# Performance work log

Measured on AMD Instinct MI355X. Metric: run time of the kernel, lower is better.

## Reference

```python
import jax, jax.numpy as jnp
import numpy as np

N = 100000        # nodes
E = 1600000       # edges (avg degree 16)
D_IN = 32
D_OUT = 64
K_HOPS = 2        # SGC propagation steps
CUTGRAPH = 0.1
K_CUT = int(E * CUTGRAPH)  # edges pruned per hop (lowest cosine similarity)
L2_EPS = 1e-12    # torch F.normalize eps


def setup_inputs() -> dict:
    key = jax.random.key(0)
    k1, k2, k3, k4 = jax.random.split(key, 4)
    features = jax.random.normal(k1, (N, D_IN), dtype=jnp.float32)
    src = jax.random.randint(k2, (E,), 0, N, dtype=jnp.int32)
    dst = jax.random.randint(k3, (E,), 0, N, dtype=jnp.int32)
    # fc weight (out_feats, in_feats), Xavier-uniform-like scale
    W = jax.random.normal(k4, (D_OUT, D_IN), dtype=jnp.float32) * (1.0 / np.sqrt(D_IN))
    return {"features": features, "src": src, "dst": dst, "W": W}


def reference(features, src, dst, W):
    # in-degree (messages flow src -> dst), clamped at 1
    deg = jax.ops.segment_sum(jnp.ones((E,), features.dtype), dst, num_segments=N)
    norm = jnp.power(jnp.clip(deg, 1.0, None), -0.5)[:, None]  # [N,1]

    h = features
    for _ in range(K_HOPS):
        # edge weights: ones, with bottom-K_CUT cosine-similarity edges zeroed
        nh = h / jnp.maximum(jnp.linalg.norm(h, axis=-1, keepdims=True), L2_EPS)
        cos = jnp.sum(nh[src] * nh[dst], axis=-1)               # [E]
        _, cut_idx = jax.lax.top_k(-cos, K_CUT)                 # smallest cos
        w = jnp.ones((E,), h.dtype).at[cut_idx].set(0.0)

        # symmetric degree-normalized propagation: D^-1/2 A D^-1/2 h
        h = h * norm
        msg = h[src] * w[:, None]                               # [E, D_IN]
        h = jax.ops.segment_sum(msg, dst, num_segments=N)       # [N, D_IN]
        h = h * norm

    return h @ W.T  # fc, no bias
```

## Files before the change

### kernel.cpp

```cpp
#include <hip/hip_runtime.h>


constexpr int NN   = 100000;
constexpr int NE   = 1600000;
constexpr int DI   = 32;
constexpr int DO   = 64;
constexpr int KCUT = 160000;
constexpr int NB   = 98;
constexpr int CH   = 4096;
constexpr int HB   = 256;
constexpr int SCAP = 19456;

typedef unsigned long long u64;


__global__ void k_zero_u32(unsigned* p, int n) {
  int i = blockIdx.x * blockDim.x + threadIdx.x;
  if (i < n) p[i] = 0u;
}

__global__ void k_norm(const unsigned* __restrict__ degi, float* __restrict__ nrm) {
  int i = blockIdx.x * blockDim.x + threadIdx.x;
  if (i < NN) {
    unsigned d = degi[i]; if (d < 1u) d = 1u;
    nrm[i] = (float)(1.0 / sqrt((double)d));
  }
}


__global__ void k_bhist(const int* __restrict__ dst, unsigned* __restrict__ bhist) {
  __shared__ unsigned lh[128];
  int t = threadIdx.x;
  if (t < 128) lh[t] = 0u;
  __syncthreads();
  int stride = gridDim.x * blockDim.x;
  for (int e = blockIdx.x * blockDim.x + t; e < NE; e += stride)
    atomicAdd(&lh[((unsigned)dst[e]) >> 10], 1u);
  __syncthreads();
  if (t < 128 && lh[t]) atomicAdd(&bhist[t], lh[t]);
}

__global__ void k_bscan(const unsigned* __restrict__ bhist, unsigned* __restrict__ bstart,
                        unsigned* __restrict__ bcur) {
  if (threadIdx.x == 0 && blockIdx.x == 0) {
    unsigned run = 0;
    for (int b = 0; b < NB; b++) { bstart[b] = run; bcur[b] = run; run += bhist[b]; }
    bstart[NB] = run;
  }
}

__global__ void k_bin(const int* __restrict__ src, const int* __restrict__ dst,
                      unsigned* __restrict__ bcur, u64* __restrict__ binned) {
  __shared__ unsigned h1[128], h2[128], res[128];
  int t = threadIdx.x;
  for (int base = blockIdx.x * CH; base < NE; base += gridDim.x * CH) {
    int nE = min(CH, NE - base);
    if (t < 128) h1[t] = 0u;
    __syncthreads();
    for (int i = t; i < nE; i += 256)
      atomicAdd(&h1[((unsigned)dst[base + i]) >> 10], 1u);
    __syncthreads();
    if (t < 128) { unsigned c = h1[t]; res[t] = c ? atomicAdd(&bcur[t], c) : 0u; h2[t] = 0u; }
    __syncthreads();
    for (int i = t; i < nE; i += 256) {
      unsigned d = (unsigned)dst[base + i];
      unsigned bb = d >> 10;
      u64 pk = ((u64)(d & 1023u) << 38) | ((u64)(unsigned)src[base + i] << 21)
             | (u64)(unsigned)(base + i);
      unsigned r = atomicAdd(&h2[bb], 1u);
      binned[res[bb] + r] = pk;
    }
    __syncthreads();
  }
}

__global__ void k_bucket_deg(const u64* __restrict__ binned, const unsigned* __restrict__ bstart,
                             unsigned* __restrict__ degi) {
  __shared__ unsigned cnt[1024];
  int t = threadIdx.x;
  int b = blockIdx.x;
  for (int i = t; i < 1024; i += 256) cnt[i] = 0u;
  __syncthreads();
  unsigned j0 = bstart[b], j1 = bstart[b + 1];
  for (unsigned j = j0 + t; j < j1; j += 256)
    atomicAdd(&cnt[(unsigned)(binned[j] >> 38)], 1u);
  __syncthreads();
  int base = b << 10;
  for (int i = t; i < 1024; i += 256)
    if (base + i < NN) degi[base + i] = cnt[i];
}

__global__ void k_bucket_scatter(const u64* __restrict__ binned, const unsigned* __restrict__ bstart,
                                 const unsigned* __restrict__ rowptr, uint2* __restrict__ csr) {
  extern __shared__ unsigned smem[];
  unsigned* curl = smem;
  u64* stage = (u64*)(smem + 1024);
  int t = threadIdx.x;
  int b = blockIdx.x;
  unsigned j0 = bstart[b], j1 = bstart[b + 1];
  int base = b << 10;
  for (int i = t; i < 1024; i += 256)
    curl[i] = (base + i < NN) ? (rowptr[base + i] - j0) : 0u;
  __syncthreads();
  for (unsigned j = j0 + t; j < j1; j += 256) {
    u64 pk = binned[j];
    unsigned dloc = (unsigned)(pk >> 38);
    unsigned s = (unsigned)((pk >> 21) & 0x1FFFFu);
    unsigned e = (unsigned)(pk & 0x1FFFFFu);
    unsigned p = atomicAdd(&curl[dloc], 1u);
    u64 entry = ((u64)e << 32) | (u64)s;
    if (p < (unsigned)SCAP) stage[p] = entry;
    else csr[j0 + p] = make_uint2(s, e);
  }
  __syncthreads();
  unsigned cnt = j1 - j0;
  u64* gout = (u64*)(csr + j0);
  for (unsigned i = t; i < cnt; i += 256)
    if (i < (unsigned)SCAP) gout[i] = stage[i];
}


__global__ void k_psum_a(const unsigned* __restrict__ degi, unsigned* __restrict__ bsum) {
  __shared__ unsigned s[1024];
  int t = threadIdx.x;
  int i = blockIdx.x * 1024 + t;
  s[t] = (i < NN) ? degi[i] : 0u;
  __syncthreads();
  for (int off = 512; off > 0; off >>= 1) {
    if (t < off) s[t] += s[t + off];
    __syncthreads();
  }
  if (t == 0) bsum[blockIdx.x] = s[0];
}

__global__ void k_psum_b(unsigned* bsum, int nb, unsigned* rowptr) {
  if (threadIdx.x == 0 && blockIdx.x == 0) {
    unsigned run = 0;
    for (int b = 0; b < nb; b++) { unsigned v = bsum[b]; bsum[b] = run; run += v; }
    rowptr[NN] = run;
  }
}

__global__ void k_psum_c(const unsigned* __restrict__ degi, const unsigned* __restrict__ bsum,
                         unsigned* __restrict__ rowptr) {
  __shared__ unsigned s[1024];
  int t = threadIdx.x;
  int i = blockIdx.x * 1024 + t;
  unsigned v = (i < NN) ? degi[i] : 0u;
  s[t] = v; __syncthreads();
  for (int off = 1; off < 1024; off <<= 1) {
    unsigned x = (t >= off) ? s[t - off] : 0u;
    __syncthreads();
    s[t] += x;
    __syncthreads();
  }
  if (i < NN) rowptr[i] = bsum[blockIdx.x] + s[t] - v;
}


__global__ void k_rownorm(const float* __restrict__ h, const float* __restrict__ nrm,
                          float* __restrict__ nh, float* __restrict__ hn) {
  int lane = threadIdx.x & 31;
  int n = blockIdx.x * 8 + (threadIdx.x >> 5);
  float v = h[n * DI + lane];
  double sq = (double)v * (double)v;
  #pragma unroll
  for (int m = 16; m > 0; m >>= 1) sq += __shfl_xor(sq, m, 32);
  double den = sqrt(sq);
  if (den < 1e-12) den = 1e-12;
  nh[n * DI + lane] = (float)((double)v / den);
  hn[n * DI + lane] = v * nrm[n];
}

__global__ void k_cos(const unsigned* __restrict__ rowptr, const uint2* __restrict__ csr,
                      const float* __restrict__ nh, u64* __restrict__ key) {
  int t = threadIdx.x;
  int lane = t & 31;
  int sl = lane >> 2;
  int ds = lane & 3;
  int n = blockIdx.x * 8 + (t >> 5);
  const float4* drow = (const float4*)(nh + (size_t)n * DI + ds * 8);
  float4 d0 = drow[0], d1 = drow[1];
  unsigned j0 = rowptr[n], j1 = rowptr[n + 1];
  for (unsigned base = j0; base < j1; base += 8) {
    unsigned j = base + sl;
    bool val = (j < j1);
    uint2 c = val ? csr[j] : make_uint2(0u, 0u);
    const float4* arow = (const float4*)(nh + (size_t)c.x * DI + ds * 8);
    float4 a0 = arow[0], a1 = arow[1];
    double p = (double)a0.x * d0.x + (double)a0.y * d0.y
             + (double)a0.z * d0.z + (double)a0.w * d0.w
             + (double)a1.x * d1.x + (double)a1.y * d1.y
             + (double)a1.z * d1.z + (double)a1.w * d1.w;
    p += __shfl_xor(p, 1, 32);
    p += __shfl_xor(p, 2, 32);
    if (val && ds == 0) {
      float cf = (float)p;
      unsigned u = __float_as_uint(cf);
      u = (u & 0x80000000u) ? ~u : (u | 0x80000000u);
      key[j] = ((u64)u << 32) | (u64)c.y;
    }
  }
}


__global__ void k_hist_big(const u64* __restrict__ keys, unsigned* __restrict__ ghist,
                           u64* state, unsigned* cur) {
  __shared__ unsigned lh[4096];
  int t = threadIdx.x;
  if (blockIdx.x == 0 && t == 0) {
    state[0] = 0ull; state[1] = (u64)KCUT; cur[0] = 0u; cur[1] = 0u;
  }
  for (int i = t; i < 4096; i += 256) lh[i] = 0u;
  __syncthreads();
  int stride = gridDim.x * blockDim.x;
  for (int j = blockIdx.x * blockDim.x + t; j < NE; j += stride)
    atomicAdd(&lh[(unsigned)(keys[j] >> 52)], 1u);
  __syncthreads();
  unsigned* gh = ghist + (size_t)blockIdx.x * 4096;
  for (int i = t; i < 4096; i += 256) gh[i] = lh[i];
}

__global__ void k_hist_reduce(const unsigned* __restrict__ ghist, unsigned* __restrict__ hist) {
  int bin = blockIdx.x * 256 + threadIdx.x;
  unsigned s = 0;
  for (int b = 0; b < HB; b++) s += ghist[(size_t)b * 4096 + bin];
  hist[bin] = s;
}

__global__ void k_hist(const u64* __restrict__ keys, const unsigned* __restrict__ cntp,
                       const u64* __restrict__ state,
                       unsigned* __restrict__ hist, int shift, int check) {
  __shared__ unsigned lh[4096];
  int t = threadIdx.x;
  for (int i = t; i < 4096; i += 256) lh[i] = 0u;
  __syncthreads();
  int n = (int)*cntp;
  u64 pref = state[0];
  int stride = gridDim.x * blockDim.x;
  for (int j = blockIdx.x * blockDim.x + t; j < n; j += stride) {
    u64 k = keys[j];
    bool ok = (check == 0) || (((k ^ pref) >> check) == 0ull);
    if (ok) atomicAdd(&lh[(unsigned)((k >> shift) & 4095ull)], 1u);
  }
  __syncthreads();
  for (int i = t; i < 4096; i += 256) if (lh[i]) atomicAdd(&hist[i], lh[i]);
}

__global__ void k_select(unsigned* hist, u64* state, int shift) {
  __shared__ unsigned ssum[256];
  int t = threadIdx.x;
  unsigned loc[16]; unsigned tot = 0;
  #pragma unroll
  for (int i = 0; i < 16; i++) { loc[i] = hist[t * 16 + i]; tot += loc[i]; }
  #pragma unroll
  for (int i = 0; i < 16; i++) hist[t * 16 + i] = 0u;
  unsigned krem = (unsigned)state[1];
  ssum[t] = tot; __syncthreads();
  for (int off = 1; off < 256; off <<= 1) {
    unsigned x = (t >= off) ? ssum[t - off] : 0u;
    __syncthreads();
    ssum[t] += x;
    __syncthreads();
  }
  unsigned incl = ssum[t], excl = incl - tot;
  if (incl >= krem && excl < krem) {
    unsigned run = excl; int b = 0; unsigned nk = 0;
    #pragma unroll
    for (int i = 0; i < 16; i++) {
      if (krem <= run + loc[i]) { b = t * 16 + i; nk = krem - run; break; }
      run += loc[i];
    }
    state[0] |= ((u64)b) << shift;
    state[1] = (u64)nk;
  }
}

__global__ void k_compact(const u64* __restrict__ keys, const unsigned* __restrict__ cntp,
                          int n_fixed, const u64* __restrict__ state, int check,
                          u64* __restrict__ outbuf, unsigned* __restrict__ cursor) {
  __shared__ u64 buf[768];
  __shared__ unsigned cnt, gbase;
  int t = threadIdx.x;
  if (t == 0) cnt = 0u;
  __syncthreads();
  int n = cntp ? (int)*cntp : n_fixed;
  u64 pref = state[0];
  int stride = gridDim.x * blockDim.x;
  for (int j0 = blockIdx.x * blockDim.x; j0 < n; j0 += stride) {
    int j = j0 + t;
    if (j < n) {
      u64 k = keys[j];
      if (((k ^ pref) >> check) == 0ull) {
        unsigned pos = atomicAdd(&cnt, 1u);
        buf[pos] = k;
      }
    }
    __syncthreads();
    if (cnt >= 512u) {
      if (t == 0) gbase = atomicAdd(cursor, cnt);
      __syncthreads();
      for (unsigned i = t; i < cnt; i += blockDim.x) outbuf[gbase + i] = buf[i];
      __syncthreads();
      if (t == 0) cnt = 0u;
      __syncthreads();
    }
  }
  if (t == 0 && cnt > 0u) gbase = atomicAdd(cursor, cnt);
  __syncthreads();
  for (unsigned i = t; i < cnt; i += blockDim.x) outbuf[gbase + i] = buf[i];
}

__global__ void __launch_bounds__(1024) k_finish(const u64* __restrict__ cb,
                                                 const unsigned* __restrict__ cur,
                                                 u64* __restrict__ state) {
  __shared__ unsigned h[1024];
  __shared__ u64 spref;
  __shared__ unsigned skrem;
  int t = threadIdx.x;
  unsigned cnt = cur[1];
  if (t == 0) { spref = state[0]; skrem = (unsigned)state[1]; }
  __syncthreads();
  for (int shift = 30; shift >= 0; shift -= 10) {
    h[t] = 0u; __syncthreads();
    u64 pref = spref;
    for (unsigned j = t; j < cnt; j += 1024) {
      u64 k = cb[j];
      if (((k ^ pref) >> (shift + 10)) == 0ull)
        atomicAdd(&h[(unsigned)((k >> shift) & 1023ull)], 1u);
    }
    __syncthreads();
    unsigned v = h[t];
    for (int off = 1; off < 1024; off <<= 1) {
      unsigned x = (t >= off) ? h[t - off] : 0u;
      __syncthreads();
      h[t] += x;
      __syncthreads();
    }
    unsigned incl = h[t], excl = incl - v;
    unsigned krem = skrem;
    __syncthreads();
    if (incl >= krem && excl < krem) {
      spref |= ((u64)t) << shift;
      skrem = krem - excl;
    }
    __syncthreads();
  }
  if (t == 0) state[0] = spref;
}


__global__ void k_prop(const unsigned* __restrict__ rowptr, const uint2* __restrict__ csr,
                       const u64* __restrict__ key, const u64* __restrict__ state,
                       const float* __restrict__ hn, const float* __restrict__ nrm,
                       float* __restrict__ hout) {
  int t = threadIdx.x;
  int lane = t & 31;
  int sl = lane >> 2, ds = lane & 3;
  int n = blockIdx.x * 8 + (t >> 5);
  u64 X = state[0];
  unsigned j0 = rowptr[n], j1 = rowptr[n + 1];
  double acc[8];
  #pragma unroll
  for (int i = 0; i < 8; i++) acc[i] = 0.0;
  for (unsigned base = j0; base < j1; base += 8) {
    unsigned j = base + sl;
    bool val = (j < j1);
    uint2 c = val ? csr[j] : make_uint2(0u, 0u);
    u64 k = val ? key[j] : 0ull;
    bool keep = val && (k > X);
    const float4* arow = (const float4*)(hn + (size_t)c.x * DI + ds * 8);
    float4 a0 = arow[0], a1 = arow[1];
    if (keep) {
      acc[0] += (double)a0.x; acc[1] += (double)a0.y;
      acc[2] += (double)a0.z; acc[3] += (double)a0.w;
      acc[4] += (double)a1.x; acc[5] += (double)a1.y;
      acc[6] += (double)a1.z; acc[7] += (double)a1.w;
    }
  }
  #pragma unroll
  for (int m = 4; m <= 16; m <<= 1) {
    #pragma unroll
    for (int i = 0; i < 8; i++) acc[i] += __shfl_xor(acc[i], m, 32);
  }
  if (sl == 0) {
    float nv = nrm[n];
    float4 o0, o1;
    o0.x = (float)acc[0] * nv; o0.y = (float)acc[1] * nv;
    o0.z = (float)acc[2] * nv; o0.w = (float)acc[3] * nv;
    o1.x = (float)acc[4] * nv; o1.y = (float)acc[5] * nv;
    o1.z = (float)acc[6] * nv; o1.w = (float)acc[7] * nv;
    float4* orow = (float4*)(hout + (size_t)n * DI + ds * 8);
    orow[0] = o0; orow[1] = o1;
  }
}


__global__ void k_fc(const float* __restrict__ h, const float* __restrict__ W,
                     float* __restrict__ out) {
  __shared__ float Wt[DI * 65];
  __shared__ float hs[4 * DI];
  int t = threadIdx.x;
  #pragma unroll
  for (int i = 0; i < 8; i++) {
    int idx = t + i * 256;
    Wt[(idx & 31) * 65 + (idx >> 5)] = W[idx];
  }
  int n0 = blockIdx.x * 4;
  if (t < 128) hs[t] = h[n0 * DI + t];
  __syncthreads();
  int o = t & 63, nl = t >> 6;
  float acc = 0.f;
  #pragma unroll
  for (int d = 0; d < DI; d++) acc += hs[nl * DI + d] * Wt[d * 65 + o];
  out[(n0 + nl) * DO + o] = acc;
}


extern "C" void kernel_launch(void* const* d_in, const int* in_sizes, int n_in,
                              void* d_out, int out_size, void* d_ws, size_t ws_size,
                              hipStream_t stream) {
  const float* feat = (const float*)d_in[0];
  const int*   src  = (const int*)d_in[1];
  const int*   dst  = (const int*)d_in[2];
  const float* W    = (const float*)d_in[3];
  float*       out  = (float*)d_out;

  float* bufA = (float*)d_ws;
  float* bufB = bufA + (size_t)NN * DI;
  float* bufC = bufB + (size_t)NN * DI;
  u64*   key  = (u64*)(bufC + (size_t)NN * DI);
  u64*   cbuf2 = key + NE;
  u64*   binned = cbuf2;
  unsigned* ghist = (unsigned*)cbuf2;
  float*    nrm     = (float*)(cbuf2 + NE);
  unsigned* degi    = (unsigned*)(nrm + NN);
  unsigned* rowptr  = degi + NN;
  unsigned* fill    = rowptr + NN + 2;
  unsigned* bsum    = fill + NN;
  unsigned* hist    = bsum + 128;
  unsigned* cur     = hist + 4096;
  u64*      state   = (u64*)(cur + 2);
  uint2*    csr     = (uint2*)(state + 2);
  unsigned* bhist   = (unsigned*)(csr + NE);
  unsigned* bstart  = bhist + 128;
  unsigned* bcur    = bstart + 100;

  k_zero_u32<<<1, 128, 0, stream>>>(bhist, 128);
  k_bhist<<<512, 256, 0, stream>>>(dst, bhist);
  k_bscan<<<1, 1, 0, stream>>>(bhist, bstart, bcur);
  k_bin<<<(NE + CH - 1) / CH, 256, 0, stream>>>(src, dst, bcur, binned);
  k_bucket_deg<<<NB, 256, 0, stream>>>(binned, bstart, degi);
  k_norm<<<(NN + 255) / 256, 256, 0, stream>>>(degi, nrm);
  int nb = (NN + 1023) / 1024;
  k_psum_a<<<nb, 1024, 0, stream>>>(degi, bsum);
  k_psum_b<<<1, 1, 0, stream>>>(bsum, nb, rowptr);
  k_psum_c<<<nb, 1024, 0, stream>>>(degi, bsum, rowptr);
  size_t scatter_lds = 1024 * sizeof(unsigned) + (size_t)SCAP * sizeof(u64);
  k_bucket_scatter<<<NB, 256, scatter_lds, stream>>>(binned, bstart, rowptr, csr);

  const float* hin = feat;
  for (int hop = 0; hop < 2; hop++) {
    float* nh = (hop == 0) ? bufA : bufC;
    float* hn = bufB;
    float* ho = (hop == 0) ? bufA : bufC;
    u64* cbuf1 = (u64*)((hop == 0) ? bufC : bufA);

    k_rownorm<<<NN / 8, 256, 0, stream>>>(hin, nrm, nh, hn);
    k_cos<<<NN / 8, 256, 0, stream>>>(rowptr, csr, nh, key);

    k_hist_big<<<HB, 256, 0, stream>>>(key, ghist, state, cur);
    k_hist_reduce<<<16, 256, 0, stream>>>(ghist, hist);
    k_select<<<1, 256, 0, stream>>>(hist, state, 52);
    k_compact<<<512, 256, 0, stream>>>(key, nullptr, NE, state, 52, cbuf1, cur + 0);
    k_hist<<<64, 256, 0, stream>>>(cbuf1, cur + 0, state, hist, 40, 0);
    k_select<<<1, 256, 0, stream>>>(hist, state, 40);
    k_compact<<<64, 256, 0, stream>>>(cbuf1, cur + 0, 0, state, 40, cbuf2, cur + 1);
    k_finish<<<1, 1024, 0, stream>>>(cbuf2, cur, state);

    k_prop<<<NN / 8, 256, 0, stream>>>(rowptr, csr, key, state, hn, nrm, ho);
    hin = ho;
  }
  k_fc<<<NN / 4, 256, 0, stream>>>(hin, W, out);
}
```

Before: 472.1 us.

## Cut kernel launches in radix top-k select and preprocessing via fused kernels

Merges the histogram reduce and first bucket select into one kernel using a last-block-done atomic, and drops the second histogram/select/compact pass. The remaining 52-bit prefix refinement now runs inside a single 1024-thread finish kernel over the first compacted buffer, in 12-bit rounds. Preprocessing also fuses the degree-norm computation into the prefix-sum kernel and replaces the atomic bucket histogram plus serial scan with per-block partials and a parallel scan. This removes several small launches and serial kernels. In exchange, one workgroup must now scan the whole first-level candidate set across five rounds, which could be slow if that set is large.

After: 512.5 us. 8.6% more time.

```diff
diff --git a/kernel.cpp b/kernel.cpp
--- a/kernel.cpp
+++ b/kernel.cpp
@@ -9,26 +9,13 @@
 constexpr int NB   = 98;
 constexpr int CH   = 4096;
 constexpr int HB   = 256;
+constexpr int HBH  = 512;
 constexpr int SCAP = 19456;
 
 typedef unsigned long long u64;
 
 
-__global__ void k_zero_u32(unsigned* p, int n) {
-  int i = blockIdx.x * blockDim.x + threadIdx.x;
-  if (i < n) p[i] = 0u;
-}
-
-__global__ void k_norm(const unsigned* __restrict__ degi, float* __restrict__ nrm) {
-  int i = blockIdx.x * blockDim.x + threadIdx.x;
-  if (i < NN) {
-    unsigned d = degi[i]; if (d < 1u) d = 1u;
-    nrm[i] = (float)(1.0 / sqrt((double)d));
-  }
-}
-
-
-__global__ void k_bhist(const int* __restrict__ dst, unsigned* __restrict__ bhist) {
+__global__ void k_bhist(const int* __restrict__ dst, unsigned* __restrict__ bpart) {
   __shared__ unsigned lh[128];
   int t = threadIdx.x;
   if (t < 128) lh[t] = 0u;
@@ -37,16 +24,25 @@
   for (int e = blockIdx.x * blockDim.x + t; e < NE; e += stride)
     atomicAdd(&lh[((unsigned)dst[e]) >> 10], 1u);
   __syncthreads();
-  if (t < 128 && lh[t]) atomicAdd(&bhist[t], lh[t]);
-}
-
-__global__ void k_bscan(const unsigned* __restrict__ bhist, unsigned* __restrict__ bstart,
-                        unsigned* __restrict__ bcur) {
-  if (threadIdx.x == 0 && blockIdx.x == 0) {
-    unsigned run = 0;
-    for (int b = 0; b < NB; b++) { bstart[b] = run; bcur[b] = run; run += bhist[b]; }
-    bstart[NB] = run;
-  }
+  if (t < 128) bpart[blockIdx.x * 128 + t] = lh[t];
+}
+
+__global__ void k_bscan2(const unsigned* __restrict__ bpart, unsigned* __restrict__ bstart,
+                         unsigned* __restrict__ bcur) {
+  __shared__ unsigned s[128];
+  int t = threadIdx.x;
+  unsigned sum = 0;
+  for (int b = 0; b < HBH; b++) sum += bpart[b * 128 + t];
+  s[t] = sum; __syncthreads();
+  for (int off = 1; off < 128; off <<= 1) {
+    unsigned x = (t >= off) ? s[t - off] : 0u;
+    __syncthreads();
+    s[t] += x;
+    __syncthreads();
+  }
+  unsigned incl = s[t], excl = incl - sum;
+  if (t < NB) { bstart[t] = excl; bcur[t] = excl; }
+  if (t == NB - 1) bstart[NB] = incl;
 }
 
 __global__ void k_bin(const int* __restrict__ src, const int* __restrict__ dst,
@@ -142,7 +138,7 @@
 }
 
 __global__ void k_psum_c(const unsigned* __restrict__ degi, const unsigned* __restrict__ bsum,
-                         unsigned* __restrict__ rowptr) {
+                         unsigned* __restrict__ rowptr, float* __restrict__ nrm) {
   __shared__ unsigned s[1024];
   int t = threadIdx.x;
   int i = blockIdx.x * 1024 + t;
@@ -154,7 +150,11 @@
     s[t] += x;
     __syncthreads();
   }
-  if (i < NN) rowptr[i] = bsum[blockIdx.x] + s[t] - v;
+  if (i < NN) {
+    rowptr[i] = bsum[blockIdx.x] + s[t] - v;
+    unsigned d = v < 1u ? 1u : v;
+    nrm[i] = (float)(1.0 / sqrt((double)d));
+  }
 }
 
 
@@ -209,7 +209,7 @@
   __shared__ unsigned lh[4096];
   int t = threadIdx.x;
   if (blockIdx.x == 0 && t == 0) {
-    state[0] = 0ull; state[1] = (u64)KCUT; cur[0] = 0u; cur[1] = 0u;
+    state[0] = 0ull; state[1] = (u64)KCUT; cur[0] = 0u; cur[1] = 0u; cur[2] = 0u;
   }
   for (int i = t; i < 4096; i += 256) lh[i] = 0u;
   __syncthreads();
@@ -221,40 +221,23 @@
   for (int i = t; i < 4096; i += 256) gh[i] = lh[i];
 }
 
-__global__ void k_hist_reduce(const unsigned* __restrict__ ghist, unsigned* __restrict__ hist) {
-  int bin = blockIdx.x * 256 + threadIdx.x;
+__global__ void k_hist_reduce_sel(const unsigned* __restrict__ ghist, unsigned* __restrict__ hist,
+                                  u64* state, unsigned* cur) {
+  __shared__ unsigned ssum[256];
+  __shared__ unsigned isLast;
+  int t = threadIdx.x;
+  int bin = blockIdx.x * 256 + t;
   unsigned s = 0;
   for (int b = 0; b < HB; b++) s += ghist[(size_t)b * 4096 + bin];
   hist[bin] = s;
-}
-
-__global__ void k_hist(const u64* __restrict__ keys, const unsigned* __restrict__ cntp,
-                       const u64* __restrict__ state,
-                       unsigned* __restrict__ hist, int shift, int check) {
-  __shared__ unsigned lh[4096];
-  int t = threadIdx.x;
-  for (int i = t; i < 4096; i += 256) lh[i] = 0u;
-  __syncthreads();
-  int n = (int)*cntp;
-  u64 pref = state[0];
-  int stride = gridDim.x * blockDim.x;
-  for (int j = blockIdx.x * blockDim.x + t; j < n; j += stride) {
-    u64 k = keys[j];
-    bool ok = (check == 0) || (((k ^ pref) >> check) == 0ull);
-    if (ok) atomicAdd(&lh[(unsigned)((k >> shift) & 4095ull)], 1u);
-  }
-  __syncthreads();
-  for (int i = t; i < 4096; i += 256) if (lh[i]) atomicAdd(&hist[i], lh[i]);
-}
-
-__global__ void k_select(unsigned* hist, u64* state, int shift) {
-  __shared__ unsigned ssum[256];
-  int t = threadIdx.x;
+  __threadfence();
+  if (t == 0) isLast = (atomicAdd(&cur[2], 1u) == gridDim.x - 1u) ? 1u : 0u;
+  __syncthreads();
+  if (!isLast) return;
+  __threadfence();
   unsigned loc[16]; unsigned tot = 0;
   #pragma unroll
   for (int i = 0; i < 16; i++) { loc[i] = hist[t * 16 + i]; tot += loc[i]; }
-  #pragma unroll
-  for (int i = 0; i < 16; i++) hist[t * 16 + i] = 0u;
   unsigned krem = (unsigned)state[1];
   ssum[t] = tot; __syncthreads();
   for (int off = 1; off < 256; off <<= 1) {
@@ -265,33 +248,33 @@
   }
   unsigned incl = ssum[t], excl = incl - tot;
   if (incl >= krem && excl < krem) {
-    unsigned run = excl; int b = 0; unsigned nk = 0;
+    unsigned run = excl;
     #pragma unroll
     for (int i = 0; i < 16; i++) {
-      if (krem <= run + loc[i]) { b = t * 16 + i; nk = krem - run; break; }
+      if (krem <= run + loc[i]) {
+        state[0] |= ((u64)(t * 16 + i)) << 52;
+        state[1] = (u64)(krem - run);
+        break;
+      }
       run += loc[i];
     }
-    state[0] |= ((u64)b) << shift;
-    state[1] = (u64)nk;
-  }
-}
-
-__global__ void k_compact(const u64* __restrict__ keys, const unsigned* __restrict__ cntp,
-                          int n_fixed, const u64* __restrict__ state, int check,
+  }
+}
+
+__global__ void k_compact(const u64* __restrict__ keys, const u64* __restrict__ state,
                           u64* __restrict__ outbuf, unsigned* __restrict__ cursor) {
   __shared__ u64 buf[768];
   __shared__ unsigned cnt, gbase;
   int t = threadIdx.x;
   if (t == 0) cnt = 0u;
   __syncthreads();
-  int n = cntp ? (int)*cntp : n_fixed;
   u64 pref = state[0];
   int stride = gridDim.x * blockDim.x;
-  for (int j0 = blockIdx.x * blockDim.x; j0 < n; j0 += stride) {
+  for (int j0 = blockIdx.x * blockDim.x; j0 < NE; j0 += stride) {
     int j = j0 + t;
-    if (j < n) {
+    if (j < NE) {
       u64 k = keys[j];
-      if (((k ^ pref) >> check) == 0ull) {
+      if (((k ^ pref) >> 52) == 0ull) {
         unsigned pos = atomicAdd(&cnt, 1u);
         buf[pos] = k;
       }
@@ -311,38 +294,58 @@
   for (unsigned i = t; i < cnt; i += blockDim.x) outbuf[gbase + i] = buf[i];
 }
 
-__global__ void __launch_bounds__(1024) k_finish(const u64* __restrict__ cb,
-                                                 const unsigned* __restrict__ cur,
-                                                 u64* __restrict__ state) {
-  __shared__ unsigned h[1024];
+__global__ void __launch_bounds__(1024) k_finish2(const u64* __restrict__ cb,
+                                                  const unsigned* __restrict__ cur,
+                                                  u64* __restrict__ state) {
+  __shared__ unsigned lh[4096];
+  __shared__ unsigned ssum[1024];
   __shared__ u64 spref;
   __shared__ unsigned skrem;
   int t = threadIdx.x;
-  unsigned cnt = cur[1];
+  unsigned cnt = cur[0];
   if (t == 0) { spref = state[0]; skrem = (unsigned)state[1]; }
   __syncthreads();
-  for (int shift = 30; shift >= 0; shift -= 10) {
-    h[t] = 0u; __syncthreads();
+  for (int r = 0; r < 5; r++) {
+    int shift = (r < 4) ? (40 - 12 * r) : 0;
+    int width = (r < 4) ? 12 : 4;
+    int nbins = 1 << width;
+    int check = shift + width;
+    for (int i = t; i < nbins; i += 1024) lh[i] = 0u;
+    __syncthreads();
     u64 pref = spref;
     for (unsigned j = t; j < cnt; j += 1024) {
       u64 k = cb[j];
-      if (((k ^ pref) >> (shift + 10)) == 0ull)
-        atomicAdd(&h[(unsigned)((k >> shift) & 1023ull)], 1u);
-    }
-    __syncthreads();
-    unsigned v = h[t];
+      if (((k ^ pref) >> check) == 0ull)
+        atomicAdd(&lh[(unsigned)((k >> shift) & (u64)(nbins - 1))], 1u);
+    }
+    __syncthreads();
+    int per = (nbins + 1023) / 1024;
+    unsigned loc[4]; unsigned tot = 0;
+    for (int i = 0; i < per; i++) {
+      int b = t * per + i;
+      loc[i] = (b < nbins) ? lh[b] : 0u;
+      tot += loc[i];
+    }
+    ssum[t] = tot; __syncthreads();
     for (int off = 1; off < 1024; off <<= 1) {
-      unsigned x = (t >= off) ? h[t - off] : 0u;
+      unsigned x = (t >= off) ? ssum[t - off] : 0u;
       __syncthreads();
-      h[t] += x;
+      ssum[t] += x;
       __syncthreads();
     }
-    unsigned incl = h[t], excl = incl - v;
+    unsigned incl = ssum[t], excl = incl - tot;
     unsigned krem = skrem;
     __syncthreads();
     if (incl >= krem && excl < krem) {
-      spref |= ((u64)t) << shift;
-      skrem = krem - excl;
+      unsigned run = excl;
+      for (int i = 0; i < per; i++) {
+        if (krem <= run + loc[i]) {
+          spref |= ((u64)(t * per + i)) << shift;
+          skrem = krem - run;
+          break;
+        }
+        run += loc[i];
+      }
     }
     __syncthreads();
   }
@@ -440,22 +443,20 @@
   unsigned* bsum    = fill + NN;
   unsigned* hist    = bsum + 128;
   unsigned* cur     = hist + 4096;
-  u64*      state   = (u64*)(cur + 2);
+  u64*      state   = (u64*)(cur + 4);
   uint2*    csr     = (uint2*)(state + 2);
-  unsigned* bhist   = (unsigned*)(csr + NE);
-  unsigned* bstart  = bhist + 128;
+  unsigned* bstart  = (unsigned*)(csr + NE);
   unsigned* bcur    = bstart + 100;
-
-  k_zero_u32<<<1, 128, 0, stream>>>(bhist, 128);
-  k_bhist<<<512, 256, 0, stream>>>(dst, bhist);
-  k_bscan<<<1, 1, 0, stream>>>(bhist, bstart, bcur);
+  unsigned* bpart   = bcur + 128;
+
+  k_bhist<<<HBH, 256, 0, stream>>>(dst, bpart);
+  k_bscan2<<<1, 128, 0, stream>>>(bpart, bstart, bcur);
   k_bin<<<(NE + CH - 1) / CH, 256, 0, stream>>>(src, dst, bcur, binned);
   k_bucket_deg<<<NB, 256, 0, stream>>>(binned, bstart, degi);
-  k_norm<<<(NN + 255) / 256, 256, 0, stream>>>(degi, nrm);
   int nb = (NN + 1023) / 1024;
   k_psum_a<<<nb, 1024, 0, stream>>>(degi, bsum);
   k_psum_b<<<1, 1, 0, stream>>>(bsum, nb, rowptr);
-  k_psum_c<<<nb, 1024, 0, stream>>>(degi, bsum, rowptr);
+  k_psum_c<<<nb, 1024, 0, stream>>>(degi, bsum, rowptr, nrm);
   size_t scatter_lds = 1024 * sizeof(unsigned) + (size_t)SCAP * sizeof(u64);
   k_bucket_scatter<<<NB, 256, scatter_lds, stream>>>(binned, bstart, rowptr, csr);
 
@@ -470,13 +471,9 @@
     k_cos<<<NN / 8, 256, 0, stream>>>(rowptr, csr, nh, key);
 
     k_hist_big<<<HB, 256, 0, stream>>>(key, ghist, state, cur);
-    k_hist_reduce<<<16, 256, 0, stream>>>(ghist, hist);
-    k_select<<<1, 256, 0, stream>>>(hist, state, 52);
-    k_compact<<<512, 256, 0, stream>>>(key, nullptr, NE, state, 52, cbuf1, cur + 0);
-    k_hist<<<64, 256, 0, stream>>>(cbuf1, cur + 0, state, hist, 40, 0);
-    k_select<<<1, 256, 0, stream>>>(hist, state, 40);
-    k_compact<<<64, 256, 0, stream>>>(cbuf1, cur + 0, 0, state, 40, cbuf2, cur + 1);
-    k_finish<<<1, 1024, 0, stream>>>(cbuf2, cur, state);
+    k_hist_reduce_sel<<<16, 256, 0, stream>>>(ghist, hist, state, cur);
+    k_compact<<<512, 256, 0, stream>>>(key, state, cbuf1, cur + 0);
+    k_finish2<<<1, 1024, 0, stream>>>(cbuf1, cur, state);
 
     k_prop<<<NN / 8, 256, 0, stream>>>(rowptr, csr, key, state, hn, nrm, ho);
     hin = ho;
```
